# Kernel optimization log

Measured on AMD Instinct MI355X. Metric: run time of the kernel, lower is better.

## Reference

```python
import jax, jax.numpy as jnp
import numpy as np
from jax import lax

B, T, V, E, H, L = 512, 128, 128, 512, 512, 2  # batch, seq, vocab, embd, hidden, layers


def setup_inputs() -> dict:
    key = jax.random.key(0)
    ks = jax.random.split(key, 6)
    s = 1.0 / np.sqrt(H)
    return {
        "input": jax.random.randint(ks[0], (B, T), 0, V),
        "encoder_curr_state": jnp.zeros((L, B, H), dtype=jnp.float32),
        "emb": jax.random.normal(ks[1], (V, E), dtype=jnp.float32) * 0.02,
        "w_ih": jax.random.uniform(ks[2], (L, 3 * H, E), minval=-s, maxval=s, dtype=jnp.float32),
        "w_hh": jax.random.uniform(ks[3], (L, 3 * H, H), minval=-s, maxval=s, dtype=jnp.float32),
        "b_ih": jax.random.uniform(ks[4], (L, 3 * H), minval=-s, maxval=s, dtype=jnp.float32),
        "b_hh": jax.random.uniform(ks[5], (L, 3 * H), minval=-s, maxval=s, dtype=jnp.float32),
    }


def _gru_cell(x, h, wi, wh, bi, bh):
    # torch GRU gate math: gates ordered (r, z, n)
    gi = x @ wi.T + bi  # [B, 3H]
    gh = h @ wh.T + bh  # [B, 3H]
    i_r, i_z, i_n = jnp.split(gi, 3, axis=-1)
    h_r, h_z, h_n = jnp.split(gh, 3, axis=-1)
    r = jax.nn.sigmoid(i_r + h_r)
    z = jax.nn.sigmoid(i_z + h_z)
    n = jnp.tanh(i_n + r * h_n)
    return (1.0 - z) * n + z * h


def reference(input, encoder_curr_state, emb, w_ih, w_hh, b_ih, b_hh):
    x_seq = emb[input]                      # [B, T, E]
    x_tbe = jnp.swapaxes(x_seq, 0, 1)       # [T, B, E]

    def step(h, x_t):
        hs = []
        inp = x_t
        for l in range(L):  # small fixed layer loop
            hl = _gru_cell(inp, h[l], w_ih[l], w_hh[l], b_ih[l], b_hh[l])
            hs.append(hl)
            inp = hl
        h_new = jnp.stack(hs)               # [L, B, H]
        return h_new, h_new

    h_final, states = lax.scan(step, encoder_curr_state, x_tbe)
    # states: [T, L, B, H] == encoder_states; h_final == encoder_curr_state after loop
    return states, h_final
```

## Files before the change

kernel.cpp:

```cpp
#include <hip/hip_runtime.h>
#include <hip/hip_bf16.h>
#include <math.h>


#define BB 512
#define TT 128
#define VV 128
#define EE 512
#define HH 512
#define LL 2
#define BH (BB*HH)

#define NBLK 192

typedef short s16x8 __attribute__((ext_vector_type(8)));
typedef float f32x4 __attribute__((ext_vector_type(4)));

typedef const __attribute__((address_space(1))) unsigned int* gptr_t;
typedef __attribute__((address_space(3))) unsigned int* lptr_t;

#define W_SZ    (3*HH*EE)
#define WH0_OFF 0
#define WI1_OFF (W_SZ)
#define WH1_OFF (2*W_SZ)
#define HBF_OFF (3*W_SZ)
#define HBF_SZ  (4*BH)
#define TBL_BYTE ((size_t)(3*W_SZ + HBF_SZ)*2)
#define TBL_SZ   (VV*3*HH)
#define BAR_BYTE (TBL_BYTE + (size_t)TBL_SZ*4)

#define MFMA(a,b,c) __builtin_amdgcn_mfma_f32_16x16x32_bf16((a),(b),(c),0,0,0)

__global__ __launch_bounds__(256) void f32_to_bf16(
    const float* __restrict__ src, __hip_bfloat16* __restrict__ dst, int n)
{
    int i = blockIdx.x * 256 + threadIdx.x;
    if (i < n) dst[i] = __float2bfloat16(src[i]);
}

__global__ __launch_bounds__(256) void build_gi0(
    const float* __restrict__ emb, const float* __restrict__ w_ih,
    const float* __restrict__ b_ih, float* __restrict__ tbl)
{
    __shared__ __align__(16) float e[EE];
    const int v   = blockIdx.y;
    const int col = blockIdx.x * 256 + threadIdx.x;
    for (int i = threadIdx.x; i < EE; i += 256) e[i] = emb[v * EE + i];
    __syncthreads();
    const float4* w4 = (const float4*)(w_ih + (size_t)col * EE);
    const float4* e4 = (const float4*)e;
    float acc = 0.f;
    #pragma unroll 8
    for (int k = 0; k < EE/4; ++k) {
        float4 wv = w4[k], ev = e4[k];
        acc += wv.x*ev.x + wv.y*ev.y + wv.z*ev.z + wv.w*ev.w;
    }
    tbl[v * (3*HH) + col] = acc + b_ih[col];
}

__device__ __forceinline__ void gl_lds16(const void* g, void* l) {
    __builtin_amdgcn_global_load_lds((gptr_t)g, (lptr_t)l, 16, 0, 0);
}

__device__ __forceinline__ s16x8 frag_ld(const __hip_bfloat16* tb, int row, int kb) {
    const char* p = (const char*)tb + row * 256 + (((kb ^ (row & 7)) & 15) << 4);
    return *(const s16x8*)p;
}

__device__ __forceinline__ float sigm(float x) { return 1.f / (1.f + __expf(-x)); }
__device__ __forceinline__ float tanh_f(float x) {
    float e2 = __expf(2.f * x);
    return 1.f - 2.f / (e2 + 1.f);
}

__device__ __forceinline__ void grid_sync(unsigned* bar) {
    __syncthreads();
    if (threadIdx.x == 0) {
        unsigned* cnt = bar;
        unsigned* gen = bar + 32;
        unsigned* abt = bar + 64;
        if (__hip_atomic_load(abt, __ATOMIC_RELAXED, __HIP_MEMORY_SCOPE_AGENT) == 0u) {
            unsigned g = __hip_atomic_load(gen, __ATOMIC_RELAXED, __HIP_MEMORY_SCOPE_AGENT);
            unsigned a = __hip_atomic_fetch_add(cnt, 1u, __ATOMIC_RELEASE, __HIP_MEMORY_SCOPE_AGENT);
            if (a == (unsigned)(NBLK - 1)) {
                __hip_atomic_store(cnt, 0u, __ATOMIC_RELAXED, __HIP_MEMORY_SCOPE_AGENT);
                __hip_atomic_store(gen, g + 1u, __ATOMIC_RELEASE, __HIP_MEMORY_SCOPE_AGENT);
            } else {
                int spins = 0;
                while (__hip_atomic_load(gen, __ATOMIC_RELAXED, __HIP_MEMORY_SCOPE_AGENT) == g) {
                    if (__hip_atomic_load(abt, __ATOMIC_RELAXED, __HIP_MEMORY_SCOPE_AGENT) != 0u)
                        break;
                    __builtin_amdgcn_s_sleep(2);
                    if (++spins > (1 << 20)) {
                        __hip_atomic_store(abt, 1u, __ATOMIC_RELAXED, __HIP_MEMORY_SCOPE_AGENT);
                        break;
                    }
                }
            }
        }
        __threadfence();
    }
    __syncthreads();
}

__global__ __launch_bounds__(512) void gru_persist(
    const int*   __restrict__ input,
    const float* __restrict__ h0,
    const float* __restrict__ b_ih,
    const float* __restrict__ b_hh,
    const __hip_bfloat16* __restrict__ wh0,
    const __hip_bfloat16* __restrict__ wi1,
    const __hip_bfloat16* __restrict__ wh1,
    const float* __restrict__ tbl,
    __hip_bfloat16* __restrict__ hbf,
    float*       __restrict__ out,
    unsigned*    __restrict__ bar)
{
    __shared__ __align__(16) __hip_bfloat16 smem[32768];
    __hip_bfloat16* As = smem;
    __hip_bfloat16* Bs = smem + 8192;

    const int tid  = threadIdx.x;
    const int w    = tid >> 6;
    const int lane = tid & 63;
    const int l15  = lane & 15;
    const int lg   = lane >> 4;
    const int bid  = blockIdx.x;

    if (bid < 64) {
        const int bt = bid >> 3, ht = bid & 7;
        const int wq = w >> 2,  hq = w & 3;

        int aoff[2], boff[6];
        #pragma unroll
        for (int i = 0; i < 2; ++i) {
            int ra = w*8 + i*4 + lg;
            aoff[i] = (bt*64 + ra)*HH + ((l15 ^ (ra & 7)) << 3);
        }
        #pragma unroll
        for (int i = 0; i < 6; ++i) {
            int rb = w*24 + i*4 + lg;
            int gg = rb >> 6, hc = rb & 63;
            boff[i] = (gg*HH + ht*64 + hc)*HH + ((l15 ^ (rb & 7)) << 3);
        }
        const int arow0 = wq*32 + l15, arow1 = wq*32 + 16 + l15;
        const int brow0 = hq*16 + l15, brow1 = 64 + hq*16 + l15, brow2 = 128 + hq*16 + l15;

        const int hcol = ht*64 + hq*16 + l15;
        const float bhr = b_hh[hcol], bhz = b_hh[512 + hcol], bhn = b_hh[1024 + hcol];

        float hreg[2][4];
        #pragma unroll
        for (int s2 = 0; s2 < 2; ++s2)
            #pragma unroll
            for (int r = 0; r < 4; ++r) {
                int b = bt*64 + wq*32 + s2*16 + lg*4 + r;
                hreg[s2][r] = h0[(size_t)b*HH + hcol];
            }

        for (int t = 0; t < TT; ++t) {
            const __hip_bfloat16* Asrc = hbf + (size_t)((t + 1) & 1) * BH;
            f32x4 acc[2][3];
            #pragma unroll
            for (int s2 = 0; s2 < 2; ++s2)
                #pragma unroll
                for (int g2 = 0; g2 < 3; ++g2) acc[s2][g2] = (f32x4)(0.f);

            #pragma unroll
            for (int c = 0; c < 4; ++c) {
                const int kc = c * 128;
                #pragma unroll
                for (int i = 0; i < 2; ++i)
                    gl_lds16(Asrc + aoff[i] + kc, As + (w*8 + i*4)*128);
                #pragma unroll
                for (int i = 0; i < 6; ++i)
                    gl_lds16(wh0 + boff[i] + kc, Bs + (w*24 + i*4)*128);
                __syncthreads();
                #pragma unroll
                for (int ks = 0; ks < 4; ++ks) {
                    const int kb = ks*4 + lg;
                    s16x8 a0 = frag_ld(As, arow0, kb);
                    s16x8 a1 = frag_ld(As, arow1, kb);
                    s16x8 b0 = frag_ld(Bs, brow0, kb);
                    s16x8 b1 = frag_ld(Bs, brow1, kb);
                    s16x8 b2 = frag_ld(Bs, brow2, kb);
                    acc[0][0] = MFMA(a0, b0, acc[0][0]);  acc[1][0] = MFMA(a1, b0, acc[1][0]);
                    acc[0][1] = MFMA(a0, b1, acc[0][1]);  acc[1][1] = MFMA(a1, b1, acc[1][1]);
                    acc[0][2] = MFMA(a0, b2, acc[0][2]);  acc[1][2] = MFMA(a1, b2, acc[1][2]);
                }
                __syncthreads();
            }

            float* outp = out + (size_t)(t * 2) * BH;
            __hip_bfloat16* hw = hbf + (size_t)(t & 1) * BH;
            #pragma unroll
            for (int s2 = 0; s2 < 2; ++s2)
                #pragma unroll
                for (int r = 0; r < 4; ++r) {
                    int b = bt*64 + wq*32 + s2*16 + lg*4 + r;
                    int v = input[b*TT + t];
                    const float* tv = tbl + v*(3*HH) + hcol;
                    float rg = sigm(acc[s2][0][r] + tv[0]   + bhr);
                    float zg = sigm(acc[s2][1][r] + tv[512] + bhz);
                    float ng = tanh_f(tv[1024] + rg*(acc[s2][2][r] + bhn));
                    float hn = (1.f - zg)*ng + zg*hreg[s2][r];
                    hreg[s2][r] = hn;
                    outp[(size_t)b*HH + hcol] = hn;
                    hw[(size_t)b*HH + hcol] = __float2bfloat16(hn);
                }
            grid_sync(bar);
        }
    } else {
        const int id = bid - 64;
        const int bt = id >> 4, ht = id & 15;
        const int bq = w >> 1,  hq = w & 1;

        int aoff[2], boff[3];
        #pragma unroll
        for (int i = 0; i < 2; ++i) {
            int ra = w*8 + i*4 + lg;
            aoff[i] = (bt*64 + ra)*HH + ((l15 ^ (ra & 7)) << 3);
        }
        #pragma unroll
        for (int i = 0; i < 3; ++i) {
            int rb = w*12 + i*4 + lg;
            int gg = rb >> 5, hc = rb & 31;
            boff[i] = (gg*HH + ht*32 + hc)*HH + ((l15 ^ (rb & 7)) << 3);
        }
        const int arow  = bq*16 + l15;
        const int brow0 = hq*16 + l15, brow1 = 32 + hq*16 + l15, brow2 = 64 + hq*16 + l15;

        const int hcol = ht*32 + hq*16 + l15;
        const float bir = b_ih[1536 + hcol], biz = b_ih[1536 + 512 + hcol], bin = b_ih[1536 + 1024 + hcol];
        const float bhr = b_hh[1536 + hcol], bhz = b_hh[1536 + 512 + hcol], bhn = b_hh[1536 + 1024 + hcol];

        float hreg[4];
        #pragma unroll
        for (int r = 0; r < 4; ++r) {
            int b = bt*64 + bq*16 + lg*4 + r;
            hreg[r] = h0[(size_t)BH + (size_t)b*HH + hcol];
        }

        grid_sync(bar);
        for (int t = 0; t < TT; ++t) {
            const __hip_bfloat16* Ax = hbf + (size_t)(t & 1) * BH;
            const __hip_bfloat16* Ah = hbf + (size_t)(2 + ((t + 1) & 1)) * BH;
            f32x4 ar = (f32x4)(0.f), az = (f32x4)(0.f), ani = (f32x4)(0.f), anh = (f32x4)(0.f);

            #pragma unroll
            for (int c = 0; c < 8; ++c) {
                const __hip_bfloat16* Asrc = (c < 4) ? Ax  : Ah;
                const __hip_bfloat16* Bsrc = (c < 4) ? wi1 : wh1;
                const int kc = (c & 3) * 128;
                #pragma unroll
                for (int i = 0; i < 2; ++i)
                    gl_lds16(Asrc + aoff[i] + kc, As + (w*8 + i*4)*128);
                #pragma unroll
                for (int i = 0; i < 3; ++i)
                    gl_lds16(Bsrc + boff[i] + kc, Bs + (w*12 + i*4)*128);
                __syncthreads();
                #pragma unroll
                for (int ks = 0; ks < 4; ++ks) {
                    const int kb = ks*4 + lg;
                    s16x8 a  = frag_ld(As, arow,  kb);
                    s16x8 b0 = frag_ld(Bs, brow0, kb);
                    s16x8 b1 = frag_ld(Bs, brow1, kb);
                    s16x8 b2 = frag_ld(Bs, brow2, kb);
                    ar = MFMA(a, b0, ar);
                    az = MFMA(a, b1, az);
                    if (c < 4) ani = MFMA(a, b2, ani);
                    else       anh = MFMA(a, b2, anh);
                }
                __syncthreads();
            }

            float* outp = out + (size_t)(t * 2 + 1) * BH;
            __hip_bfloat16* hw = hbf + (size_t)(2 + (t & 1)) * BH;
            #pragma unroll
            for (int r = 0; r < 4; ++r) {
                float rg = sigm(ar[r] + bir + bhr);
                float zg = sigm(az[r] + biz + bhz);
                float ng = tanh_f(ani[r] + bin + rg*(anh[r] + bhn));
                float hn = (1.f - zg)*ng + zg*hreg[r];
                hreg[r] = hn;
                int b = bt*64 + bq*16 + lg*4 + r;
                outp[(size_t)b*HH + hcol] = hn;
                hw[(size_t)b*HH + hcol] = __float2bfloat16(hn);
            }
            if (t < TT - 1) grid_sync(bar);
        }
    }
}

__global__ __launch_bounds__(256) void copy_final(
    const float* __restrict__ states, float* __restrict__ dst)
{
    const int i = blockIdx.x * 256 + threadIdx.x;
    dst[i] = states[(size_t)(TT - 1) * LL * BH + i];
}

extern "C" void kernel_launch(void* const* d_in, const int* in_sizes, int n_in,
                              void* d_out, int out_size, void* d_ws, size_t ws_size,
                              hipStream_t stream) {
    const int*   input = (const int*)  d_in[0];
    const float* h0    = (const float*)d_in[1];
    const float* emb   = (const float*)d_in[2];
    const float* w_ih  = (const float*)d_in[3];
    const float* w_hh  = (const float*)d_in[4];
    const float* b_ih  = (const float*)d_in[5];
    const float* b_hh  = (const float*)d_in[6];
    float* out = (float*)d_out;

    __hip_bfloat16* wsb = (__hip_bfloat16*)d_ws;
    __hip_bfloat16* wh0 = wsb + WH0_OFF;
    __hip_bfloat16* wi1 = wsb + WI1_OFF;
    __hip_bfloat16* wh1 = wsb + WH1_OFF;
    __hip_bfloat16* hbf = wsb + HBF_OFF;
    float*    tbl = (float*)   ((char*)d_ws + TBL_BYTE);
    unsigned* bar = (unsigned*)((char*)d_ws + BAR_BYTE);

    hipMemsetAsync(bar, 0, 512, stream);
    f32_to_bf16<<<(W_SZ + 255)/256, 256, 0, stream>>>(w_hh,        wh0, W_SZ);
    f32_to_bf16<<<(W_SZ + 255)/256, 256, 0, stream>>>(w_ih + W_SZ, wi1, W_SZ);
    f32_to_bf16<<<(W_SZ + 255)/256, 256, 0, stream>>>(w_hh + W_SZ, wh1, W_SZ);
    f32_to_bf16<<<(BH + 255)/256, 256, 0, stream>>>(h0,      hbf + 1*(size_t)BH, BH);
    f32_to_bf16<<<(BH + 255)/256, 256, 0, stream>>>(h0 + BH, hbf + 3*(size_t)BH, BH);
    build_gi0<<<dim3(6, VV), 256, 0, stream>>>(emb, w_ih, b_ih, tbl);

    gru_persist<<<NBLK, 512, 0, stream>>>(input, h0, b_ih, b_hh,
                                          wh0, wi1, wh1, tbl, hbf, out, bar);

    copy_final<<<(LL*BH)/256, 256, 0, stream>>>(out, out + (size_t)TT * LL * BH);
}
```

Measured before the change: 2.614 ms.

## Keep GRU weights resident in LDS and split grid sync by batch group

Each persistent block now loads its slice of the recurrent (and layer-1 input) weights into 96KB of dynamic LDS once, instead of streaming them from global memory through LDS every timestep. Activations are read straight from global memory into MFMA fragments. The batch is split into 4 independent groups of 48 blocks, each with its own barrier, so a grid sync only waits on blocks in the same batch tile. Weight-conversion kernels are merged into one launch and table lookups are hoisted ahead of the MFMA loop. The cost is much higher LDS use per block, which limits occupancy, and unstaged global A-fragment loads.

```diff
diff --git a/kernel.cpp b/kernel.cpp
--- a/kernel.cpp
+++ b/kernel.cpp
@@ -12,12 +12,10 @@
 #define BH (BB*HH)
 
 #define NBLK 192
+#define GS   48
 
 typedef short s16x8 __attribute__((ext_vector_type(8)));
 typedef float f32x4 __attribute__((ext_vector_type(4)));
-
-typedef const __attribute__((address_space(1))) unsigned int* gptr_t;
-typedef __attribute__((address_space(3))) unsigned int* lptr_t;
 
 #define W_SZ    (3*HH*EE)
 #define WH0_OFF 0
@@ -31,11 +29,20 @@
 
 #define MFMA(a,b,c) __builtin_amdgcn_mfma_f32_16x16x32_bf16((a),(b),(c),0,0,0)
 
-__global__ __launch_bounds__(256) void f32_to_bf16(
-    const float* __restrict__ src, __hip_bfloat16* __restrict__ dst, int n)
+#define PREP_N (3*W_SZ + 2*BH)
+__global__ __launch_bounds__(256) void prep_bf16(
+    const float* __restrict__ w_ih, const float* __restrict__ w_hh,
+    const float* __restrict__ h0, __hip_bfloat16* __restrict__ wsb)
 {
-    int i = blockIdx.x * 256 + threadIdx.x;
-    if (i < n) dst[i] = __float2bfloat16(src[i]);
+    const int i = blockIdx.x * 256 + threadIdx.x;
+    if (i >= PREP_N) return;
+    float v; int dst;
+    if (i < W_SZ)            { v = w_hh[i];                 dst = i; }
+    else if (i < 2*W_SZ)     { v = w_ih[W_SZ + i - W_SZ];   dst = i; }
+    else if (i < 3*W_SZ)     { v = w_hh[W_SZ + i - 2*W_SZ]; dst = i; }
+    else if (i < 3*W_SZ+BH)  { v = h0[i - 3*W_SZ];          dst = HBF_OFF + BH + (i - 3*W_SZ); }
+    else                     { v = h0[i - 3*W_SZ];          dst = HBF_OFF + 3*BH + (i - 3*W_SZ - BH); }
+    wsb[dst] = __float2bfloat16(v);
 }
 
 __global__ __launch_bounds__(256) void build_gi0(
@@ -58,31 +65,23 @@
     tbl[v * (3*HH) + col] = acc + b_ih[col];
 }
 
-__device__ __forceinline__ void gl_lds16(const void* g, void* l) {
-    __builtin_amdgcn_global_load_lds((gptr_t)g, (lptr_t)l, 16, 0, 0);
-}
-
-__device__ __forceinline__ s16x8 frag_ld(const __hip_bfloat16* tb, int row, int kb) {
-    const char* p = (const char*)tb + row * 256 + (((kb ^ (row & 7)) & 15) << 4);
-    return *(const s16x8*)p;
-}
-
 __device__ __forceinline__ float sigm(float x) { return 1.f / (1.f + __expf(-x)); }
 __device__ __forceinline__ float tanh_f(float x) {
     float e2 = __expf(2.f * x);
     return 1.f - 2.f / (e2 + 1.f);
 }
 
-__device__ __forceinline__ void grid_sync(unsigned* bar) {
+__device__ __forceinline__ void grid_sync(unsigned* base) {
+    asm volatile("s_waitcnt vmcnt(0)" ::: "memory");
     __syncthreads();
     if (threadIdx.x == 0) {
-        unsigned* cnt = bar;
-        unsigned* gen = bar + 32;
-        unsigned* abt = bar + 64;
+        unsigned* cnt = base;
+        unsigned* gen = base + 32;
+        unsigned* abt = base + 64;
         if (__hip_atomic_load(abt, __ATOMIC_RELAXED, __HIP_MEMORY_SCOPE_AGENT) == 0u) {
             unsigned g = __hip_atomic_load(gen, __ATOMIC_RELAXED, __HIP_MEMORY_SCOPE_AGENT);
             unsigned a = __hip_atomic_fetch_add(cnt, 1u, __ATOMIC_RELEASE, __HIP_MEMORY_SCOPE_AGENT);
-            if (a == (unsigned)(NBLK - 1)) {
+            if (a == (unsigned)(GS - 1)) {
                 __hip_atomic_store(cnt, 0u, __ATOMIC_RELAXED, __HIP_MEMORY_SCOPE_AGENT);
                 __hip_atomic_store(gen, g + 1u, __ATOMIC_RELEASE, __HIP_MEMORY_SCOPE_AGENT);
             } else {
@@ -116,9 +115,7 @@
     float*       __restrict__ out,
     unsigned*    __restrict__ bar)
 {
-    __shared__ __align__(16) __hip_bfloat16 smem[32768];
-    __hip_bfloat16* As = smem;
-    __hip_bfloat16* Bs = smem + 8192;
+    extern __shared__ __align__(16) char lds[];
 
     const int tid  = threadIdx.x;
     const int w    = tid >> 6;
@@ -128,150 +125,135 @@
     const int bid  = blockIdx.x;
 
     if (bid < 64) {
-        const int bt = bid >> 3, ht = bid & 7;
-        const int wq = w >> 2,  hq = w & 3;
-
-        int aoff[2], boff[6];
+        const int bt = bid >> 4, ht = bid & 15;
+        unsigned* gbar = bar + bt * 128;
+        const int B0 = bt * 128 + w * 16;
+        const int hbase = ht * 32;
+
+        for (int j = 0; j < 12; ++j) {
+            int cidx = tid + 512 * j;
+            int lr = cidx >> 6, blk = cidx & 63;
+            int g = lr >> 5, hl = lr & 31;
+            s16x8 wv = *(const s16x8*)(wh0 + (size_t)(g*512 + hbase + hl)*512 + blk*8);
+            *(s16x8*)(&lds[lr*1024 + ((blk ^ (lr & 7)) << 4)]) = wv;
+        }
+        __syncthreads();
+
+        float bi_[2][3], bh_[2][3];
         #pragma unroll
-        for (int i = 0; i < 2; ++i) {
-            int ra = w*8 + i*4 + lg;
-            aoff[i] = (bt*64 + ra)*HH + ((l15 ^ (ra & 7)) << 3);
-        }
-        #pragma unroll
-        for (int i = 0; i < 6; ++i) {
-            int rb = w*24 + i*4 + lg;
-            int gg = rb >> 6, hc = rb & 63;
-            boff[i] = (gg*HH + ht*64 + hc)*HH + ((l15 ^ (rb & 7)) << 3);
-        }
-        const int arow0 = wq*32 + l15, arow1 = wq*32 + 16 + l15;
-        const int brow0 = hq*16 + l15, brow1 = 64 + hq*16 + l15, brow2 = 128 + hq*16 + l15;
-
-        const int hcol = ht*64 + hq*16 + l15;
-        const float bhr = b_hh[hcol], bhz = b_hh[512 + hcol], bhn = b_hh[1024 + hcol];
+        for (int nt = 0; nt < 2; ++nt) {
+            const int h = hbase + nt*16 + l15;
+            #pragma unroll
+            for (int g = 0; g < 3; ++g) bh_[nt][g] = b_hh[g*512 + h];
+        }
+        (void)bi_;
 
         float hreg[2][4];
         #pragma unroll
-        for (int s2 = 0; s2 < 2; ++s2)
+        for (int nt = 0; nt < 2; ++nt)
+            #pragma unroll
+            for (int r = 0; r < 4; ++r)
+                hreg[nt][r] = h0[(size_t)(B0 + lg*4 + r)*HH + hbase + nt*16 + l15];
+
+        for (int t = 0; t < TT; ++t) {
+            const __hip_bfloat16* hsrc = hbf + (size_t)((t + 1) & 1) * BH;
+
+            float tv[2][3][4];
             #pragma unroll
             for (int r = 0; r < 4; ++r) {
-                int b = bt*64 + wq*32 + s2*16 + lg*4 + r;
-                hreg[s2][r] = h0[(size_t)b*HH + hcol];
-            }
-
-        for (int t = 0; t < TT; ++t) {
-            const __hip_bfloat16* Asrc = hbf + (size_t)((t + 1) & 1) * BH;
+                int vv = input[(B0 + lg*4 + r)*TT + t];
+                const float* tp = tbl + (size_t)vv*(3*HH) + hbase + l15;
+                #pragma unroll
+                for (int g = 0; g < 3; ++g)
+                    #pragma unroll
+                    for (int nt = 0; nt < 2; ++nt)
+                        tv[nt][g][r] = tp[g*512 + nt*16];
+            }
+
             f32x4 acc[2][3];
             #pragma unroll
-            for (int s2 = 0; s2 < 2; ++s2)
+            for (int nt = 0; nt < 2; ++nt)
                 #pragma unroll
-                for (int g2 = 0; g2 < 3; ++g2) acc[s2][g2] = (f32x4)(0.f);
-
-            #pragma unroll
-            for (int c = 0; c < 4; ++c) {
-                const int kc = c * 128;
+                for (int g = 0; g < 3; ++g) acc[nt][g] = (f32x4)(0.f);
+
+            #pragma unroll
+            for (int c = 0; c < 16; ++c) {
+                const s16x8 a = *(const s16x8*)(hsrc + (size_t)(B0 + l15)*512 + c*32 + lg*8);
                 #pragma unroll
-                for (int i = 0; i < 2; ++i)
-                    gl_lds16(Asrc + aoff[i] + kc, As + (w*8 + i*4)*128);
-                #pragma unroll
-                for (int i = 0; i < 6; ++i)
-                    gl_lds16(wh0 + boff[i] + kc, Bs + (w*24 + i*4)*128);
-                __syncthreads();
-                #pragma unroll
-                for (int ks = 0; ks < 4; ++ks) {
-                    const int kb = ks*4 + lg;
-                    s16x8 a0 = frag_ld(As, arow0, kb);
-                    s16x8 a1 = frag_ld(As, arow1, kb);
-                    s16x8 b0 = frag_ld(Bs, brow0, kb);
-                    s16x8 b1 = frag_ld(Bs, brow1, kb);
-                    s16x8 b2 = frag_ld(Bs, brow2, kb);
-                    acc[0][0] = MFMA(a0, b0, acc[0][0]);  acc[1][0] = MFMA(a1, b0, acc[1][0]);
-                    acc[0][1] = MFMA(a0, b1, acc[0][1]);  acc[1][1] = MFMA(a1, b1, acc[1][1]);
-                    acc[0][2] = MFMA(a0, b2, acc[0][2]);  acc[1][2] = MFMA(a1, b2, acc[1][2]);
-                }
-                __syncthreads();
+                for (int nt = 0; nt < 2; ++nt)
+                    #pragma unroll
+                    for (int g = 0; g < 3; ++g) {
+                        int lr = g*32 + nt*16 + l15;
+                        s16x8 bf = *(const s16x8*)(&lds[lr*1024 + (((c*4 + lg) ^ (lr & 7)) << 4)]);
+                        acc[nt][g] = MFMA(a, bf, acc[nt][g]);
+                    }
             }
 
             float* outp = out + (size_t)(t * 2) * BH;
             __hip_bfloat16* hw = hbf + (size_t)(t & 1) * BH;
             #pragma unroll
-            for (int s2 = 0; s2 < 2; ++s2)
+            for (int nt = 0; nt < 2; ++nt) {
+                const int h = hbase + nt*16 + l15;
                 #pragma unroll
                 for (int r = 0; r < 4; ++r) {
-                    int b = bt*64 + wq*32 + s2*16 + lg*4 + r;
-                    int v = input[b*TT + t];
-                    const float* tv = tbl + v*(3*HH) + hcol;
-                    float rg = sigm(acc[s2][0][r] + tv[0]   + bhr);
-                    float zg = sigm(acc[s2][1][r] + tv[512] + bhz);
-                    float ng = tanh_f(tv[1024] + rg*(acc[s2][2][r] + bhn));
-                    float hn = (1.f - zg)*ng + zg*hreg[s2][r];
-                    hreg[s2][r] = hn;
-                    outp[(size_t)b*HH + hcol] = hn;
-                    hw[(size_t)b*HH + hcol] = __float2bfloat16(hn);
+                    const int b = B0 + lg*4 + r;
+                    float rg = sigm(acc[nt][0][r] + tv[nt][0][r] + bh_[nt][0]);
+                    float zg = sigm(acc[nt][1][r] + tv[nt][1][r] + bh_[nt][1]);
+                    float ng = tanh_f(tv[nt][2][r] + rg*(acc[nt][2][r] + bh_[nt][2]));
+                    float hn = (1.f - zg)*ng + zg*hreg[nt][r];
+                    hreg[nt][r] = hn;
+                    outp[(size_t)b*HH + h] = hn;
+                    hw[(size_t)b*HH + h] = __float2bfloat16(hn);
                 }
-            grid_sync(bar);
+            }
+            grid_sync(gbar);
         }
     } else {
         const int id = bid - 64;
-        const int bt = id >> 4, ht = id & 15;
-        const int bq = w >> 1,  hq = w & 1;
-
-        int aoff[2], boff[3];
-        #pragma unroll
-        for (int i = 0; i < 2; ++i) {
-            int ra = w*8 + i*4 + lg;
-            aoff[i] = (bt*64 + ra)*HH + ((l15 ^ (ra & 7)) << 3);
-        }
-        #pragma unroll
-        for (int i = 0; i < 3; ++i) {
-            int rb = w*12 + i*4 + lg;
-            int gg = rb >> 5, hc = rb & 31;
-            boff[i] = (gg*HH + ht*32 + hc)*HH + ((l15 ^ (rb & 7)) << 3);
-        }
-        const int arow  = bq*16 + l15;
-        const int brow0 = hq*16 + l15, brow1 = 32 + hq*16 + l15, brow2 = 64 + hq*16 + l15;
-
-        const int hcol = ht*32 + hq*16 + l15;
-        const float bir = b_ih[1536 + hcol], biz = b_ih[1536 + 512 + hcol], bin = b_ih[1536 + 1024 + hcol];
-        const float bhr = b_hh[1536 + hcol], bhz = b_hh[1536 + 512 + hcol], bhn = b_hh[1536 + 1024 + hcol];
+        const int bt = id >> 5, ht = id & 31;
+        unsigned* gbar = bar + bt * 128;
+        const int B0 = bt * 128 + w * 16;
+        const int hbase = ht * 16;
+
+        for (int j = 0; j < 12; ++j) {
+            int cidx = tid + 512 * j;
+            int lr = cidx >> 7, blk = cidx & 127;
+            int g = lr >> 4, hl = lr & 15;
+            const __hip_bfloat16* src = (blk < 64) ? wi1 : wh1;
+            s16x8 wv = *(const s16x8*)(src + (size_t)(g*512 + hbase + hl)*512 + (blk & 63)*8);
+            *(s16x8*)(&lds[lr*2048 + ((blk ^ (lr & 7)) << 4)]) = wv;
+        }
+        __syncthreads();
+
+        const int h = hbase + l15;
+        const float bir = b_ih[1536 + h],       biz = b_ih[1536 + 512 + h],
+                    bin = b_ih[1536 + 1024 + h];
+        const float bhr = b_hh[1536 + h],       bhz = b_hh[1536 + 512 + h],
+                    bhn = b_hh[1536 + 1024 + h];
 
         float hreg[4];
         #pragma unroll
-        for (int r = 0; r < 4; ++r) {
-            int b = bt*64 + bq*16 + lg*4 + r;
-            hreg[r] = h0[(size_t)BH + (size_t)b*HH + hcol];
-        }
-
-        grid_sync(bar);
+        for (int r = 0; r < 4; ++r)
+            hreg[r] = h0[(size_t)BH + (size_t)(B0 + lg*4 + r)*HH + h];
+
+        grid_sync(gbar);
         for (int t = 0; t < TT; ++t) {
-            const __hip_bfloat16* Ax = hbf + (size_t)(t & 1) * BH;
-            const __hip_bfloat16* Ah = hbf + (size_t)(2 + ((t + 1) & 1)) * BH;
+            const __hip_bfloat16* xsrc = hbf + (size_t)(t & 1) * BH;
+            const __hip_bfloat16* hsrc = hbf + (size_t)(2 + ((t + 1) & 1)) * BH;
             f32x4 ar = (f32x4)(0.f), az = (f32x4)(0.f), ani = (f32x4)(0.f), anh = (f32x4)(0.f);
 
             #pragma unroll
-            for (int c = 0; c < 8; ++c) {
-                const __hip_bfloat16* Asrc = (c < 4) ? Ax  : Ah;
-                const __hip_bfloat16* Bsrc = (c < 4) ? wi1 : wh1;
-                const int kc = (c & 3) * 128;
-                #pragma unroll
-                for (int i = 0; i < 2; ++i)
-                    gl_lds16(Asrc + aoff[i] + kc, As + (w*8 + i*4)*128);
-                #pragma unroll
-                for (int i = 0; i < 3; ++i)
-                    gl_lds16(Bsrc + boff[i] + kc, Bs + (w*12 + i*4)*128);
-                __syncthreads();
-                #pragma unroll
-                for (int ks = 0; ks < 4; ++ks) {
-                    const int kb = ks*4 + lg;
-                    s16x8 a  = frag_ld(As, arow,  kb);
-                    s16x8 b0 = frag_ld(Bs, brow0, kb);
-                    s16x8 b1 = frag_ld(Bs, brow1, kb);
-                    s16x8 b2 = frag_ld(Bs, brow2, kb);
-                    ar = MFMA(a, b0, ar);
-                    az = MFMA(a, b1, az);
-                    if (c < 4) ani = MFMA(a, b2, ani);
-                    else       anh = MFMA(a, b2, anh);
-                }
-                __syncthreads();
+            for (int c = 0; c < 32; ++c) {
+                const __hip_bfloat16* asrc = (c < 16) ? xsrc : hsrc;
+                const s16x8 a = *(const s16x8*)(asrc + (size_t)(B0 + l15)*512 + (c & 15)*32 + lg*8);
+                int lr0 = 0*16 + l15, lr1 = 1*16 + l15, lr2 = 2*16 + l15;
+                s16x8 b0 = *(const s16x8*)(&lds[lr0*2048 + (((c*4 + lg) ^ (lr0 & 7)) << 4)]);
+                s16x8 b1 = *(const s16x8*)(&lds[lr1*2048 + (((c*4 + lg) ^ (lr1 & 7)) << 4)]);
+                s16x8 b2 = *(const s16x8*)(&lds[lr2*2048 + (((c*4 + lg) ^ (lr2 & 7)) << 4)]);
+                ar = MFMA(a, b0, ar);
+                az = MFMA(a, b1, az);
+                if (c < 16) ani = MFMA(a, b2, ani);
+                else        anh = MFMA(a, b2, anh);
             }
 
             float* outp = out + (size_t)(t * 2 + 1) * BH;
@@ -283,11 +265,11 @@
                 float ng = tanh_f(ani[r] + bin + rg*(anh[r] + bhn));
                 float hn = (1.f - zg)*ng + zg*hreg[r];
                 hreg[r] = hn;
-                int b = bt*64 + bq*16 + lg*4 + r;
-                outp[(size_t)b*HH + hcol] = hn;
-                hw[(size_t)b*HH + hcol] = __float2bfloat16(hn);
-            }
-            if (t < TT - 1) grid_sync(bar);
+                int b = B0 + lg*4 + r;
+                outp[(size_t)b*HH + h] = hn;
+                hw[(size_t)b*HH + h] = __float2bfloat16(hn);
+            }
+            if (t < TT - 1) grid_sync(gbar);
         }
     }
 }
@@ -319,16 +301,12 @@
     float*    tbl = (float*)   ((char*)d_ws + TBL_BYTE);
     unsigned* bar = (unsigned*)((char*)d_ws + BAR_BYTE);
 
-    hipMemsetAsync(bar, 0, 512, stream);
-    f32_to_bf16<<<(W_SZ + 255)/256, 256, 0, stream>>>(w_hh,        wh0, W_SZ);
-    f32_to_bf16<<<(W_SZ + 255)/256, 256, 0, stream>>>(w_ih + W_SZ, wi1, W_SZ);
-    f32_to_bf16<<<(W_SZ + 255)/256, 256, 0, stream>>>(w_hh + W_SZ, wh1, W_SZ);
-    f32_to_bf16<<<(BH + 255)/256, 256, 0, stream>>>(h0,      hbf + 1*(size_t)BH, BH);
-    f32_to_bf16<<<(BH + 255)/256, 256, 0, stream>>>(h0 + BH, hbf + 3*(size_t)BH, BH);
+    hipMemsetAsync(bar, 0, 2048, stream);
+    prep_bf16<<<(PREP_N + 255)/256, 256, 0, stream>>>(w_ih, w_hh, h0, wsb);
     build_gi0<<<dim3(6, VV), 256, 0, stream>>>(emb, w_ih, b_ih, tbl);
 
-    gru_persist<<<NBLK, 512, 0, stream>>>(input, h0, b_ih, b_hh,
-                                          wh0, wi1, wh1, tbl, hbf, out, bar);
+    gru_persist<<<NBLK, 512, 98304, stream>>>(input, h0, b_ih, b_hh,
+                                              wh0, wi1, wh1, tbl, hbf, out, bar);
 
     copy_final<<<(LL*BH)/256, 256, 0, stream>>>(out, out + (size_t)TT * LL * BH);
 }
```

Result: slower. 2.682 ms (+2.6%).
